# Performance work log

Measured on AMD Instinct MI355X. Metric: run time of the kernel, lower is better.

## Reference

```python
import jax, jax.numpy as jnp
import numpy as np

K_SIZE = 3
SCALE = 4
PADDING = K_SIZE // 2


def setup_inputs() -> dict:
    key = jax.random.key(0)
    k1, k2, k3, k4 = jax.random.split(key, 4)
    B, C, H, W = 8, 3, 1024, 1024
    ho, wo = H // SCALE, W // SCALE
    img = jax.random.normal(k1, (B, C, H, W), dtype=jnp.float32)
    kernels = jax.random.uniform(k2, (B, K_SIZE * K_SIZE, ho, wo), dtype=jnp.float32)
    offsets_h = jax.random.normal(k3, (B, K_SIZE * K_SIZE, ho, wo), dtype=jnp.float32)
    offsets_v = jax.random.normal(k4, (B, K_SIZE * K_SIZE, ho, wo), dtype=jnp.float32)
    offset_unit = jnp.full((1,), 4.0, dtype=jnp.float32)
    return {"img": img, "kernels": kernels, "offsets_h": offsets_h,
            "offsets_v": offsets_v, "offset_unit": offset_unit}


def _adaptive_downsample(img, kernels, offsets_h, offsets_v, offset_unit):
    # img: [B,C,H,W]; kernels/offsets: [B,k^2,ho,wo]; offset_unit: [1]
    B, C, H, W = img.shape
    ho, wo = kernels.shape[2], kernels.shape[3]
    # reflection pad as in nn.ReflectionPad2d(padding)
    imgp = jnp.pad(img, ((0, 0), (0, 0), (PADDING, PADDING), (PADDING, PADDING)), mode="reflect")
    Hp, Wp = imgp.shape[2], imgp.shape[3]

    k = jnp.arange(K_SIZE)
    ky = jnp.repeat(k, K_SIZE).astype(jnp.float32)  # [k^2] row index of kernel tap
    kx = jnp.tile(k, K_SIZE).astype(jnp.float32)    # [k^2] col index of kernel tap

    # output-pixel centers in original image coords; +PADDING shift into padded
    # coords cancels the -PADDING tap centering, so padded sample position is
    # center + k (k in 0..k_size-1).
    cy = (jnp.arange(ho, dtype=jnp.float32) + 0.5) * SCALE - 0.5  # [ho]
    cx = (jnp.arange(wo, dtype=jnp.float32) + 0.5) * SCALE - 0.5  # [wo]

    ou = offset_unit.reshape(())
    # sample positions in padded image, shape [B, k^2, ho, wo]
    p_y = cy[None, None, :, None] + ky[None, :, None, None] + offsets_v * ou
    p_x = cx[None, None, None, :] + kx[None, :, None, None] + offsets_h * ou

    y0f = jnp.floor(p_y)
    x0f = jnp.floor(p_x)
    beta = p_y - y0f   # vertical bilinear weight
    alpha = p_x - x0f  # horizontal bilinear weight

    y0 = jnp.clip(y0f.astype(jnp.int32), 0, Hp - 1)
    y1 = jnp.clip(y0 + 1, 0, Hp - 1)
    x0 = jnp.clip(x0f.astype(jnp.int32), 0, Wp - 1)
    x1 = jnp.clip(x0 + 1, 0, Wp - 1)

    def gather(yi, xi):
        # imgp: [B,C,Hp,Wp]; yi/xi: [B,k^2,ho,wo] -> [B,C,k^2,ho,wo]
        return jax.vmap(lambda im, y, x: im[:, y, x])(imgp, yi, xi)

    v00 = gather(y0, x0)
    v01 = gather(y0, x1)
    v10 = gather(y1, x0)
    v11 = gather(y1, x1)

    a = alpha[:, None]  # [B,1,k^2,ho,wo]
    b_ = beta[:, None]
    val = ((1 - a) * (1 - b_) * v00 + a * (1 - b_) * v01 +
           (1 - a) * b_ * v10 + a * b_ * v11)  # [B,C,k^2,ho,wo]

    # per-pixel learned kernel weighted sum over the k^2 taps
    out = jnp.einsum("bckhw,bkhw->bchw", val, kernels)
    return out


def reference(img, kernels, offsets_h, offsets_v, offset_unit):
    return _adaptive_downsample(img, kernels, offsets_h, offsets_v, offset_unit)
```

## Files before the change

kernel.cpp:

```cpp
#include <hip/hip_runtime.h>
#include <cstdint>

namespace {
constexpr int B = 8, C = 3, H = 1024, W = 1024;
constexpr int HO = 256, WO = 256, K2 = 9;
constexpr int HP = H + 2, WP = W + 2;
constexpr int HW = H * W, HOWO = HO * WO;

constexpr int TW = 32, TH = 16;
constexpr int NTX = WO / TW;
constexpr int NTY = HO / TH;
constexpr int OF = 12;
constexpr int WINW = 4 * TW + 2 * OF;
constexpr int WINH = 4 * TH + 2 * OF;
constexpr int WPX = WINW * WINH;
constexpr size_t LDS_BYTES = (size_t)WPX * 12;

__device__ __forceinline__ int reflect_src(int p, int n) {
    int s = p - 1;
    s = (s < 0) ? -s : s;
    s = (s >= n) ? (2 * n - 2 - s) : s;
    return s;
}

__global__ __launch_bounds__(512) void ds_tiled(
    const float* __restrict__ img,
    const float* __restrict__ kern,
    const float* __restrict__ offh,
    const float* __restrict__ offv,
    const float* __restrict__ ou_p,
    float* __restrict__ out) {
    extern __shared__ unsigned char smem[];
    float2* __restrict__ lA = (float2*)smem;
    float*  __restrict__ lB = (float*)(smem + (size_t)WPX * 8);

    const int b   = blockIdx.x & 7;
    const int tid = threadIdx.x;
    const int t   = blockIdx.x >> 3;
    const int w0  = (t & (NTX - 1)) * TW;
    const int h0  = (t >> 3) * TH;
    const int X0  = 4 * w0 - (OF - 1);
    const int Y0  = 4 * h0 - (OF - 1);

    const float* __restrict__ p0 = img + (size_t)b * (C * HW);
    const float* __restrict__ p1 = p0 + HW;
    const float* __restrict__ p2 = p1 + HW;

    for (int i = tid; i < WPX; i += 512) {
        int yy = i / WINW;
        int xx = i - yy * WINW;
        int Yp = min(max(Y0 + yy, 0), HP - 1);
        int Xp = min(max(X0 + xx, 0), WP - 1);
        int sy = reflect_src(Yp, H);
        int sx = reflect_src(Xp, W);
        size_t si = (size_t)sy * W + sx;
        lA[i] = make_float2(p0[si], p1[si]);
        lB[i] = p2[si];
    }
    __syncthreads();

    const int lw = tid & (TW - 1);
    const int lh = tid >> 5;
    const int h = h0 + lh, w = w0 + lw;
    const float ou = ou_p[0];
    const float cy = (h + 0.5f) * 4.0f - 0.5f;
    const float cx = (w + 0.5f) * 4.0f - 0.5f;
    const size_t pb = ((size_t)b * K2) * (size_t)HOWO + (size_t)h * WO + w;

    float acc0 = 0.f, acc1 = 0.f, acc2 = 0.f;

#pragma unroll
    for (int k = 0; k < K2; ++k) {
        size_t o = pb + (size_t)(k * HOWO);
        float kv = kern[o];
        float py = cy + (float)(k / 3) + offv[o] * ou;
        float px = cx + (float)(k % 3) + offh[o] * ou;

        float y0f = floorf(py), x0f = floorf(px);
        float bb = py - y0f;
        float aa = px - x0f;

        int y0 = min(max((int)y0f, 0), HP - 1);
        int x0 = min(max((int)x0f, 0), WP - 1);
        int y1 = min(y0 + 1, HP - 1);
        int x1 = min(x0 + 1, WP - 1);

        float v00x, v00y, v00z, v01x, v01y, v01z;
        float v10x, v10y, v10z, v11x, v11y, v11z;

        bool inw = (y0 >= Y0) & (y1 <= Y0 + WINH - 1) &
                   (x0 >= X0) & (x1 <= X0 + WINW - 1);
        if (__builtin_expect(inw, 1)) {
            int i00 = (y0 - Y0) * WINW + (x0 - X0);
            int dx  = x1 - x0;
            int dyr = (y1 - y0) * WINW;
            int i01 = i00 + dx, i10 = i00 + dyr, i11 = i00 + dyr + dx;
            float2 a;
            a = lA[i00]; v00x = a.x; v00y = a.y; v00z = lB[i00];
            a = lA[i01]; v01x = a.x; v01y = a.y; v01z = lB[i01];
            a = lA[i10]; v10x = a.x; v10y = a.y; v10z = lB[i10];
            a = lA[i11]; v11x = a.x; v11y = a.y; v11z = lB[i11];
        } else {
            int sy0 = reflect_src(y0, H), sy1 = reflect_src(y1, H);
            int sx0 = reflect_src(x0, W), sx1 = reflect_src(x1, W);
            size_t i0 = (size_t)sy0 * W + sx0, i1 = (size_t)sy0 * W + sx1;
            size_t i2 = (size_t)sy1 * W + sx0, i3 = (size_t)sy1 * W + sx1;
            v00x = p0[i0]; v00y = p1[i0]; v00z = p2[i0];
            v01x = p0[i1]; v01y = p1[i1]; v01z = p2[i1];
            v10x = p0[i2]; v10y = p1[i2]; v10z = p2[i2];
            v11x = p0[i3]; v11y = p1[i3]; v11z = p2[i3];
        }

        float tx_, tu_;
        tx_ = v00x + aa * (v01x - v00x);
        tu_ = v10x + aa * (v11x - v10x);
        acc0 += kv * (tx_ + bb * (tu_ - tx_));
        tx_ = v00y + aa * (v01y - v00y);
        tu_ = v10y + aa * (v11y - v10y);
        acc1 += kv * (tx_ + bb * (tu_ - tx_));
        tx_ = v00z + aa * (v01z - v00z);
        tu_ = v10z + aa * (v11z - v10z);
        acc2 += kv * (tx_ + bb * (tu_ - tx_));
    }

    size_t obase = ((size_t)b * C) * (size_t)HOWO + (size_t)h * WO + w;
    out[obase] = acc0;
    out[obase + (size_t)HOWO] = acc1;
    out[obase + (size_t)(2 * HOWO)] = acc2;
}
}

extern "C" void kernel_launch(void* const* d_in, const int* in_sizes, int n_in,
                              void* d_out, int out_size, void* d_ws, size_t ws_size,
                              hipStream_t stream) {
    const float* img  = (const float*)d_in[0];
    const float* kern = (const float*)d_in[1];
    const float* offh = (const float*)d_in[2];
    const float* offv = (const float*)d_in[3];
    const float* ou   = (const float*)d_in[4];
    float* out = (float*)d_out;

    static bool attr_set = false;
    if (!attr_set) {
        hipFuncSetAttribute(reinterpret_cast<const void*>(&ds_tiled),
                            hipFuncAttributeMaxDynamicSharedMemorySize,
                            (int)LDS_BYTES);
        attr_set = true;
    }

    hipLaunchKernelGGL(ds_tiled, dim3(B * NTX * NTY), dim3(512), LDS_BYTES,
                       stream, img, kern, offh, offv, ou, out);
}
```

Measured before the change: 241.7 us.

## Split work per channel into separate blocks with smaller static LDS windows

```diff
diff --git a/kernel.cpp b/kernel.cpp
--- a/kernel.cpp
+++ b/kernel.cpp
@@ -10,11 +10,11 @@
 constexpr int TW = 32, TH = 16;
 constexpr int NTX = WO / TW;
 constexpr int NTY = HO / TH;
+constexpr int NT  = NTX * NTY;
 constexpr int OF = 12;
 constexpr int WINW = 4 * TW + 2 * OF;
 constexpr int WINH = 4 * TH + 2 * OF;
 constexpr int WPX = WINW * WINH;
-constexpr size_t LDS_BYTES = (size_t)WPX * 12;
 
 __device__ __forceinline__ int reflect_src(int p, int n) {
     int s = p - 1;
@@ -23,28 +23,26 @@
     return s;
 }
 
-__global__ __launch_bounds__(512) void ds_tiled(
+__global__ __launch_bounds__(512, 6) void ds_split(
     const float* __restrict__ img,
     const float* __restrict__ kern,
     const float* __restrict__ offh,
     const float* __restrict__ offv,
     const float* __restrict__ ou_p,
     float* __restrict__ out) {
-    extern __shared__ unsigned char smem[];
-    float2* __restrict__ lA = (float2*)smem;
-    float*  __restrict__ lB = (float*)(smem + (size_t)WPX * 8);
+    __shared__ float win[WPX];
 
-    const int b   = blockIdx.x & 7;
-    const int tid = threadIdx.x;
-    const int t   = blockIdx.x >> 3;
-    const int w0  = (t & (NTX - 1)) * TW;
-    const int h0  = (t >> 3) * TH;
-    const int X0  = 4 * w0 - (OF - 1);
-    const int Y0  = 4 * h0 - (OF - 1);
+    const int b    = blockIdx.x & 7;
+    const int rest = blockIdx.x >> 3;
+    const int c    = rest % 3;
+    const int t    = rest / 3;
+    const int tid  = threadIdx.x;
+    const int w0   = (t & (NTX - 1)) * TW;
+    const int h0   = (t >> 3) * TH;
+    const int X0   = 4 * w0 - (OF - 1);
+    const int Y0   = 4 * h0 - (OF - 1);
 
-    const float* __restrict__ p0 = img + (size_t)b * (C * HW);
-    const float* __restrict__ p1 = p0 + HW;
-    const float* __restrict__ p2 = p1 + HW;
+    const float* __restrict__ p = img + ((size_t)b * C + c) * (size_t)HW;
 
     for (int i = tid; i < WPX; i += 512) {
         int yy = i / WINW;
@@ -53,9 +51,7 @@
         int Xp = min(max(X0 + xx, 0), WP - 1);
         int sy = reflect_src(Yp, H);
         int sx = reflect_src(Xp, W);
-        size_t si = (size_t)sy * W + sx;
-        lA[i] = make_float2(p0[si], p1[si]);
-        lB[i] = p2[si];
+        win[i] = p[(size_t)sy * W + sx];
     }
     __syncthreads();
 
@@ -67,7 +63,7 @@
     const float cx = (w + 0.5f) * 4.0f - 0.5f;
     const size_t pb = ((size_t)b * K2) * (size_t)HOWO + (size_t)h * WO + w;
 
-    float acc0 = 0.f, acc1 = 0.f, acc2 = 0.f;
+    float acc = 0.f;
 
 #pragma unroll
     for (int k = 0; k < K2; ++k) {
@@ -85,48 +81,32 @@
         int y1 = min(y0 + 1, HP - 1);
         int x1 = min(x0 + 1, WP - 1);
 
-        float v00x, v00y, v00z, v01x, v01y, v01z;
-        float v10x, v10y, v10z, v11x, v11y, v11z;
-
+        float v00, v01, v10, v11;
         bool inw = (y0 >= Y0) & (y1 <= Y0 + WINH - 1) &
                    (x0 >= X0) & (x1 <= X0 + WINW - 1);
         if (__builtin_expect(inw, 1)) {
             int i00 = (y0 - Y0) * WINW + (x0 - X0);
             int dx  = x1 - x0;
             int dyr = (y1 - y0) * WINW;
-            int i01 = i00 + dx, i10 = i00 + dyr, i11 = i00 + dyr + dx;
-            float2 a;
-            a = lA[i00]; v00x = a.x; v00y = a.y; v00z = lB[i00];
-            a = lA[i01]; v01x = a.x; v01y = a.y; v01z = lB[i01];
-            a = lA[i10]; v10x = a.x; v10y = a.y; v10z = lB[i10];
-            a = lA[i11]; v11x = a.x; v11y = a.y; v11z = lB[i11];
+            v00 = win[i00];
+            v01 = win[i00 + dx];
+            v10 = win[i00 + dyr];
+            v11 = win[i00 + dyr + dx];
         } else {
             int sy0 = reflect_src(y0, H), sy1 = reflect_src(y1, H);
             int sx0 = reflect_src(x0, W), sx1 = reflect_src(x1, W);
-            size_t i0 = (size_t)sy0 * W + sx0, i1 = (size_t)sy0 * W + sx1;
-            size_t i2 = (size_t)sy1 * W + sx0, i3 = (size_t)sy1 * W + sx1;
-            v00x = p0[i0]; v00y = p1[i0]; v00z = p2[i0];
-            v01x = p0[i1]; v01y = p1[i1]; v01z = p2[i1];
-            v10x = p0[i2]; v10y = p1[i2]; v10z = p2[i2];
-            v11x = p0[i3]; v11y = p1[i3]; v11z = p2[i3];
+            v00 = p[(size_t)sy0 * W + sx0];
+            v01 = p[(size_t)sy0 * W + sx1];
+            v10 = p[(size_t)sy1 * W + sx0];
+            v11 = p[(size_t)sy1 * W + sx1];
         }
 
-        float tx_, tu_;
-        tx_ = v00x + aa * (v01x - v00x);
-        tu_ = v10x + aa * (v11x - v10x);
-        acc0 += kv * (tx_ + bb * (tu_ - tx_));
-        tx_ = v00y + aa * (v01y - v00y);
-        tu_ = v10y + aa * (v11y - v10y);
-        acc1 += kv * (tx_ + bb * (tu_ - tx_));
-        tx_ = v00z + aa * (v01z - v00z);
-        tu_ = v10z + aa * (v11z - v10z);
-        acc2 += kv * (tx_ + bb * (tu_ - tx_));
+        float tx_ = v00 + aa * (v01 - v00);
+        float tu_ = v10 + aa * (v11 - v10);
+        acc += kv * (tx_ + bb * (tu_ - tx_));
     }
 
-    size_t obase = ((size_t)b * C) * (size_t)HOWO + (size_t)h * WO + w;
-    out[obase] = acc0;
-    out[obase + (size_t)HOWO] = acc1;
-    out[obase + (size_t)(2 * HOWO)] = acc2;
+    out[((size_t)b * C + c) * (size_t)HOWO + (size_t)h * WO + w] = acc;
 }
 }
 
@@ -140,14 +120,6 @@
     const float* ou   = (const float*)d_in[4];
     float* out = (float*)d_out;
 
-    static bool attr_set = false;
-    if (!attr_set) {
-        hipFuncSetAttribute(reinterpret_cast<const void*>(&ds_tiled),
-                            hipFuncAttributeMaxDynamicSharedMemorySize,
-                            (int)LDS_BYTES);
-        attr_set = true;
-    }
-
-    hipLaunchKernelGGL(ds_tiled, dim3(B * NTX * NTY), dim3(512), LDS_BYTES,
-                       stream, img, kern, offh, offv, ou, out);
+    hipLaunchKernelGGL(ds_split, dim3(B * NT * C), dim3(512), 0, stream,
+                       img, kern, offh, offv, ou, out);
 }
```

Result: slower. 277.9 us (+15.0%).

## Vectorize LDS window fill and prefetch per-pixel kernel/offset loads before staging

Applied to the files above, without the earlier changes.

```diff
diff --git a/kernel.cpp b/kernel.cpp
--- a/kernel.cpp
+++ b/kernel.cpp
@@ -10,11 +10,16 @@
 constexpr int TW = 32, TH = 16;
 constexpr int NTX = WO / TW;
 constexpr int NTY = HO / TH;
+constexpr int NT  = NTX * NTY;
 constexpr int OF = 12;
 constexpr int WINW = 4 * TW + 2 * OF;
 constexpr int WINH = 4 * TH + 2 * OF;
-constexpr int WPX = WINW * WINH;
-constexpr size_t LDS_BYTES = (size_t)WPX * 12;
+constexpr int WPX  = WINW * WINH;
+constexpr int CPR  = WINW / 4;
+constexpr int CHPP = CPR * WINH;
+
+constexpr size_t LA_BYTES  = (size_t)(WPX + 2) * 8;
+constexpr size_t LDS_BYTES = LA_BYTES + (size_t)(WPX + 1) * 4;
 
 __device__ __forceinline__ int reflect_src(int p, int n) {
     int s = p - 1;
@@ -23,7 +28,7 @@
     return s;
 }
 
-__global__ __launch_bounds__(512) void ds_tiled(
+__global__ __launch_bounds__(512) void ds_fused(
     const float* __restrict__ img,
     const float* __restrict__ kern,
     const float* __restrict__ offh,
@@ -32,11 +37,11 @@
     float* __restrict__ out) {
     extern __shared__ unsigned char smem[];
     float2* __restrict__ lA = (float2*)smem;
-    float*  __restrict__ lB = (float*)(smem + (size_t)WPX * 8);
+    float*  __restrict__ lB = (float*)(smem + LA_BYTES);
 
     const int b   = blockIdx.x & 7;
+    const int t   = blockIdx.x >> 3;
     const int tid = threadIdx.x;
-    const int t   = blockIdx.x >> 3;
     const int w0  = (t & (NTX - 1)) * TW;
     const int h0  = (t >> 3) * TH;
     const int X0  = 4 * w0 - (OF - 1);
@@ -46,35 +51,74 @@
     const float* __restrict__ p1 = p0 + HW;
     const float* __restrict__ p2 = p1 + HW;
 
-    for (int i = tid; i < WPX; i += 512) {
-        int yy = i / WINW;
-        int xx = i - yy * WINW;
-        int Yp = min(max(Y0 + yy, 0), HP - 1);
-        int Xp = min(max(X0 + xx, 0), WP - 1);
-        int sy = reflect_src(Yp, H);
-        int sx = reflect_src(Xp, W);
-        size_t si = (size_t)sy * W + sx;
-        lA[i] = make_float2(p0[si], p1[si]);
-        lB[i] = p2[si];
-    }
-    __syncthreads();
-
     const int lw = tid & (TW - 1);
     const int lh = tid >> 5;
     const int h = h0 + lh, w = w0 + lw;
+    const int pb = (b * K2) * HOWO + h * WO + w;
+    float kv[K2], vv[K2], hh[K2];
+#pragma unroll
+    for (int k = 0; k < K2; ++k) {
+        kv[k] = kern[pb + k * HOWO];
+        vv[k] = offv[pb + k * HOWO];
+        hh[k] = offh[pb + k * HOWO];
+    }
     const float ou = ou_p[0];
+
+    for (int i = tid; i < CHPP; i += 512) {
+        int yy = i / CPR, xc = i - yy * CPR;
+        int Yp = min(max(Y0 + yy, 0), HP - 1);
+        int sy = reflect_src(Yp, H);
+        int gx = X0 - 1 + 4 * xc;
+        float4 a0, a1;
+        if (gx >= 0 && gx <= W - 4) {
+            a0 = *(const float4*)(p0 + (size_t)sy * W + gx);
+            a1 = *(const float4*)(p1 + (size_t)sy * W + gx);
+        } else {
+            float t0[4], t1[4];
+#pragma unroll
+            for (int j = 0; j < 4; ++j) {
+                int Xp = min(max(X0 + 4 * xc + j, 0), WP - 1);
+                int sx = reflect_src(Xp, W);
+                t0[j] = p0[(size_t)sy * W + sx];
+                t1[j] = p1[(size_t)sy * W + sx];
+            }
+            a0 = make_float4(t0[0], t0[1], t0[2], t0[3]);
+            a1 = make_float4(t1[0], t1[1], t1[2], t1[3]);
+        }
+        float4* dst = (float4*)(lA + 4 * i);
+        dst[0] = make_float4(a0.x, a1.x, a0.y, a1.y);
+        dst[1] = make_float4(a0.z, a1.z, a0.w, a1.w);
+    }
+    for (int i = tid; i < CHPP; i += 512) {
+        int yy = i / CPR, xc = i - yy * CPR;
+        int Yp = min(max(Y0 + yy, 0), HP - 1);
+        int sy = reflect_src(Yp, H);
+        int gx = X0 - 1 + 4 * xc;
+        float4 a2;
+        if (gx >= 0 && gx <= W - 4) {
+            a2 = *(const float4*)(p2 + (size_t)sy * W + gx);
+        } else {
+            float t2[4];
+#pragma unroll
+            for (int j = 0; j < 4; ++j) {
+                int Xp = min(max(X0 + 4 * xc + j, 0), WP - 1);
+                int sx = reflect_src(Xp, W);
+                t2[j] = p2[(size_t)sy * W + sx];
+            }
+            a2 = make_float4(t2[0], t2[1], t2[2], t2[3]);
+        }
+        *(float4*)(lB + 4 * i) = a2;
+    }
+    __syncthreads();
+
     const float cy = (h + 0.5f) * 4.0f - 0.5f;
     const float cx = (w + 0.5f) * 4.0f - 0.5f;
-    const size_t pb = ((size_t)b * K2) * (size_t)HOWO + (size_t)h * WO + w;
-
     float acc0 = 0.f, acc1 = 0.f, acc2 = 0.f;
 
 #pragma unroll
     for (int k = 0; k < K2; ++k) {
-        size_t o = pb + (size_t)(k * HOWO);
-        float kv = kern[o];
-        float py = cy + (float)(k / 3) + offv[o] * ou;
-        float px = cx + (float)(k % 3) + offh[o] * ou;
+        float py = cy + (float)(k / 3) + vv[k] * ou;
+        float px = cx + (float)(k % 3) + hh[k] * ou;
 
         float y0f = floorf(py), x0f = floorf(px);
         float bb = py - y0f;
@@ -92,35 +136,40 @@
                    (x0 >= X0) & (x1 <= X0 + WINW - 1);
         if (__builtin_expect(inw, 1)) {
             int i00 = (y0 - Y0) * WINW + (x0 - X0);
-            int dx  = x1 - x0;
-            int dyr = (y1 - y0) * WINW;
-            int i01 = i00 + dx, i10 = i00 + dyr, i11 = i00 + dyr + dx;
-            float2 a;
-            a = lA[i00]; v00x = a.x; v00y = a.y; v00z = lB[i00];
-            a = lA[i01]; v01x = a.x; v01y = a.y; v01z = lB[i01];
-            a = lA[i10]; v10x = a.x; v10y = a.y; v10z = lB[i10];
-            a = lA[i11]; v11x = a.x; v11y = a.y; v11z = lB[i11];
+            int i10 = i00 + (y1 - y0) * WINW;
+            bool dx = (x1 > x0);
+            float2 a00 = lA[i00], a01 = lA[i00 + 1];
+            float2 a10 = lA[i10], a11 = lA[i10 + 1];
+            float  b00 = lB[i00], b01 = lB[i00 + 1];
+            float  b10 = lB[i10], b11 = lB[i10 + 1];
+            float2 s01 = dx ? a01 : a00;
+            float2 s11 = dx ? a11 : a10;
+            float  c01 = dx ? b01 : b00;
+            float  c11 = dx ? b11 : b10;
+            v00x = a00.x; v00y = a00.y; v00z = b00;
+            v01x = s01.x; v01y = s01.y; v01z = c01;
+            v10x = a10.x; v10y = a10.y; v10z = b10;
+            v11x = s11.x; v11y = s11.y; v11z = c11;
         } else {
             int sy0 = reflect_src(y0, H), sy1 = reflect_src(y1, H);
             int sx0 = reflect_src(x0, W), sx1 = reflect_src(x1, W);
             size_t i0 = (size_t)sy0 * W + sx0, i1 = (size_t)sy0 * W + sx1;
             size_t i2 = (size_t)sy1 * W + sx0, i3 = (size_t)sy1 * W + sx1;
-            v00x = p0[i0]; v00y = p1[i0]; v00z = p2[i0];
-            v01x = p0[i1]; v01y = p1[i1]; v01z = p2[i1];
-            v10x = p0[i2]; v10y = p1[i2]; v10z = p2[i2];
-            v11x = p0[i3]; v11y = p1[i3]; v11z = p2[i3];
+            v00x = p0[i0]; v01x = p0[i1]; v10x = p0[i2]; v11x = p0[i3];
+            v00y = p1[i0]; v01y = p1[i1]; v10y = p1[i2]; v11y = p1[i3];
+            v00z = p2[i0]; v01z = p2[i1]; v10z = p2[i2]; v11z = p2[i3];
         }
 
         float tx_, tu_;
         tx_ = v00x + aa * (v01x - v00x);
         tu_ = v10x + aa * (v11x - v10x);
-        acc0 += kv * (tx_ + bb * (tu_ - tx_));
+        acc0 += kv[k] * (tx_ + bb * (tu_ - tx_));
         tx_ = v00y + aa * (v01y - v00y);
         tu_ = v10y + aa * (v11y - v10y);
-        acc1 += kv * (tx_ + bb * (tu_ - tx_));
+        acc1 += kv[k] * (tx_ + bb * (tu_ - tx_));
         tx_ = v00z + aa * (v01z - v00z);
         tu_ = v10z + aa * (v11z - v10z);
-        acc2 += kv * (tx_ + bb * (tu_ - tx_));
+        acc2 += kv[k] * (tx_ + bb * (tu_ - tx_));
     }
 
     size_t obase = ((size_t)b * C) * (size_t)HOWO + (size_t)h * WO + w;
@@ -142,12 +191,12 @@
 
     static bool attr_set = false;
     if (!attr_set) {
-        hipFuncSetAttribute(reinterpret_cast<const void*>(&ds_tiled),
+        hipFuncSetAttribute(reinterpret_cast<const void*>(&ds_fused),
                             hipFuncAttributeMaxDynamicSharedMemorySize,
                             (int)LDS_BYTES);
         attr_set = true;
     }
 
-    hipLaunchKernelGGL(ds_tiled, dim3(B * NTX * NTY), dim3(512), LDS_BYTES,
-                       stream, img, kern, offh, offv, ou, out);
-}
+    hipLaunchKernelGGL(ds_fused, dim3(B * NT), dim3(512), LDS_BYTES, stream,
+                       img, kern, offh, offv, ou, out);
+}
```

Result: faster. 221.7 us (-8.3%).
